# Optimization experiments

Hardware: AMD Instinct MI355X
Metric: run time of the kernel (lower is better)

Reference implementation:

```python
import jax, jax.numpy as jnp
import numpy as np

N_NODES = 100000
N_EDGES = 1600000
N_GRAPHS = 1024
IN_CH = 64
HID = 32
H4, H2 = HID * 4, HID * 2


def _glorot(key, shape):
    fan_in, fan_out = shape[0], shape[1]
    lim = (6.0 / (fan_in + fan_out)) ** 0.5
    return jax.random.uniform(key, shape, jnp.float32, -lim, lim)


def setup_inputs() -> dict:
    key = jax.random.key(0)
    ks = jax.random.split(key, 32)
    inp = {
        "x": jax.random.normal(ks[0], (N_NODES, IN_CH), jnp.float32),
        "edge_index": jax.random.randint(ks[1], (2, N_EDGES), 0, N_NODES, jnp.int64),
        "batch": jnp.sort(jax.random.randint(ks[2], (N_NODES,), 0, N_GRAPHS, jnp.int64)),
    }
    dims = [(IN_CH, H4), (H4, H2), (H2, H2), (H2, H2)]
    for i, (di, do) in enumerate(dims, 1):
        inp[f"c{i}_wl"] = _glorot(ks[3 * i], (di, do))
        inp[f"c{i}_bl"] = jnp.zeros((do,), jnp.float32)
        inp[f"c{i}_wr"] = _glorot(ks[3 * i + 1], (di, do))
    lin_dims = [(H2, H2), (H2, HID), (HID, HID), (HID, 1)]
    for i, (di, do) in enumerate(lin_dims, 1):
        inp[f"lin{i}_w"] = _glorot(ks[15 + 2 * i], (di, do))
        inp[f"lin{i}_b"] = jnp.zeros((do,), jnp.float32)
    return inp


def _sage(x, src, dst, wl, bl, wr):
    # mean-aggregate neighbor (source) features at target nodes
    agg = jax.ops.segment_sum(x[src], dst, num_segments=N_NODES)
    deg = jax.ops.segment_sum(jnp.ones((src.shape[0],), x.dtype), dst, num_segments=N_NODES)
    agg = agg / jnp.maximum(deg, 1.0)[:, None]
    return agg @ wl + bl + x @ wr


def reference(x, edge_index, batch,
              c1_wl, c1_bl, c1_wr, c2_wl, c2_bl, c2_wr,
              c3_wl, c3_bl, c3_wr, c4_wl, c4_bl, c4_wr,
              lin1_w, lin1_b, lin2_w, lin2_b, lin3_w, lin3_b, lin4_w, lin4_b):
    src, dst = edge_index[0], edge_index[1]
    h = jax.nn.relu(_sage(x, src, dst, c1_wl, c1_bl, c1_wr))
    h = jax.nn.relu(_sage(h, src, dst, c2_wl, c2_bl, c2_wr))
    h = jax.nn.relu(_sage(h, src, dst, c3_wl, c3_bl, c3_wr))
    h = jax.nn.relu(_sage(h, src, dst, c4_wl, c4_bl, c4_wr))
    # global mean pool over graphs
    gsum = jax.ops.segment_sum(h, batch, num_segments=N_GRAPHS)
    gcnt = jax.ops.segment_sum(jnp.ones((h.shape[0],), h.dtype), batch, num_segments=N_GRAPHS)
    g = gsum / jnp.maximum(gcnt, 1.0)[:, None]
    g = jax.nn.relu(g @ lin1_w + lin1_b)
    g = jax.nn.relu(g @ lin2_w + lin2_b)
    g = jax.nn.relu(g @ lin3_w + lin3_b)
    out = (g @ lin4_w + lin4_b).squeeze(1)  # [N_GRAPHS]
    return out
```

## Files before the change

kernel.cpp:

```cpp
#include <hip/hip_runtime.h>

#define NN 100000
#define NE 1600000
#define NG 1024
#define NBLK_SCAN ((NN + 255) / 256)
#define NPART 2

#define CPAD 16

#define GB_COUNT 6250
#define GB_CVT   3125
#define GB_BND   5
#define GB_PREP  320
#define GB_SETUP (GB_COUNT + GB_CVT + GB_BND + GB_PREP)

typedef __attribute__((ext_vector_type(8))) short bf16x8;
typedef __attribute__((ext_vector_type(4))) float f32x4;

__device__ __forceinline__ unsigned f2bf1(float f) {
  union { float f; unsigned u; } v; v.f = f;
  return (v.u + 0x7fffu + ((v.u >> 16) & 1u)) >> 16;
}
__device__ __forceinline__ unsigned packbf2(float a, float b) {
  return f2bf1(a) | (f2bf1(b) << 16);
}
__device__ __forceinline__ float bflo(unsigned u) {
  union { unsigned u; float f; } v; v.u = u << 16; return v.f;
}
__device__ __forceinline__ float bfhi(unsigned u) {
  union { unsigned u; float f; } v; v.u = u & 0xffff0000u; return v.f;
}
__device__ __forceinline__ float bfs(unsigned short s) {
  union { unsigned u; float f; } v; v.u = ((unsigned)s) << 16; return v.f;
}

__global__ __launch_bounds__(256) void k_setup(
    const int* __restrict__ dst, int* __restrict__ cnt, int* __restrict__ rank,
    const float* __restrict__ X, unsigned short* __restrict__ Xb,
    const int* __restrict__ batch, int* __restrict__ gstart,
    const float* __restrict__ c1wl, const float* __restrict__ c1wr,
    const float* __restrict__ c2wl, const float* __restrict__ c2wr,
    const float* __restrict__ c3wl, const float* __restrict__ c3wr,
    const float* __restrict__ c4wl, const float* __restrict__ c4wr,
    unsigned short* __restrict__ pL1, unsigned short* __restrict__ pL2a,
    unsigned short* __restrict__ pL2b, unsigned short* __restrict__ pL3,
    unsigned short* __restrict__ pL4) {
  int b = blockIdx.x, tid = threadIdx.x;
  if (b < GB_COUNT) {
    int e = b * 256 + tid;
    rank[e] = atomicAdd(&cnt[(size_t)dst[e] * CPAD], 1);
    return;
  }
  b -= GB_COUNT;
  if (b < GB_CVT) {
    int i = b * 256 + tid;
    const float4* p = (const float4*)X + (size_t)i * 2;
    float4 a = p[0], c = p[1];
    uint4 o;
    o.x = packbf2(a.x, a.y); o.y = packbf2(a.z, a.w);
    o.z = packbf2(c.x, c.y); o.w = packbf2(c.z, c.w);
    ((uint4*)Xb)[i] = o;
    return;
  }
  b -= GB_CVT;
  if (b < GB_BND) {
    int g = b * 256 + tid;
    if (g > NG) return;
    int lo = 0, hi = NN;
    while (lo < hi) {
      int mid = (lo + hi) >> 1;
      if (batch[mid] < g) lo = mid + 1; else hi = mid;
    }
    gstart[g] = lo;
    return;
  }
  b -= GB_BND;
  {
    int yb = b >> 6, xb = b & 63;
    const float *WL, *WR; unsigned short* dstp; int N;
    if (yb == 0)      { WL = c1wl; WR = c1wr;           dstp = pL1;  N = 128; }
    else if (yb == 1) { WL = c2wl; WR = c2wl + 64 * 64; dstp = pL2a; N = 64; }
    else if (yb == 2) { WL = c2wr; WR = c2wr + 64 * 64; dstp = pL2b; N = 64; }
    else if (yb == 3) { WL = c3wl; WR = c3wr;           dstp = pL3;  N = 64; }
    else              { WL = c4wl; WR = c4wr;           dstp = pL4;  N = 64; }
    int e = xb * 256 + tid;
    if (e >= 128 * N) return;
    int k = e / N, n = e - k * N;
    float w = (k < 64) ? WL[k * N + n] : WR[(k - 64) * N + n];
    int t = k >> 5, kq = (k >> 3) & 3, j = k & 7;
    int n0 = n >> 4, nl = n & 15;
    dstp[((((n0 * 4 + t) * 64) + (kq * 16 + nl)) << 3) + j] =
        (unsigned short)f2bf1(w);
  }
}

__global__ __launch_bounds__(256) void k_scan1(const int* __restrict__ cnt,
                                               int* __restrict__ off,
                                               int* __restrict__ bsum) {
  __shared__ int s[256];
  int tid = threadIdx.x;
  int i = blockIdx.x * 256 + tid;
  int v = (i < NN) ? cnt[(size_t)i * CPAD] : 0;
  s[tid] = v;
  __syncthreads();
  for (int d = 1; d < 256; d <<= 1) {
    int t = (tid >= d) ? s[tid - d] : 0;
    __syncthreads();
    s[tid] += t;
    __syncthreads();
  }
  if (i < NN) off[i] = s[tid] - v;
  if (tid == 255) bsum[blockIdx.x] = s[255];
}

__global__ __launch_bounds__(256) void k_scan23(int* __restrict__ off,
                                                const int* __restrict__ bsum,
                                                const int* __restrict__ cnt,
                                                float* __restrict__ inv) {
  __shared__ int red[256];
  int b = blockIdx.x, tid = threadIdx.x;
  int s = 0;
  for (int j = tid; j < b; j += 256) s += bsum[j];
  red[tid] = s;
  __syncthreads();
  for (int d = 128; d > 0; d >>= 1) {
    if (tid < d) red[tid] += red[tid + d];
    __syncthreads();
  }
  int base = red[0];
  int i = b * 256 + tid;
  if (i < NN) {
    off[i] = off[i] + base;
    inv[i] = 1.0f / fmaxf((float)cnt[(size_t)i * CPAD], 1.0f);
  }
  if (i == 0) off[NN] = NE;
}

__global__ __launch_bounds__(256) void k_fill(const int* __restrict__ src,
                                              const int* __restrict__ dst,
                                              const int* __restrict__ off,
                                              const int* __restrict__ rank,
                                              int* __restrict__ csr) {
  int e = blockIdx.x * 256 + threadIdx.x;
  int lo = (int)blockIdx.y * (NN / NPART);
  int hi = lo + (NN / NPART);
  if (e < NE) {
    int d = dst[e];
    if (d >= lo && d < hi) csr[off[d] + rank[e]] = src[e];
  }
}

__global__ __launch_bounds__(256) void k_gather(
    const unsigned short* __restrict__ F, const int* __restrict__ csr,
    const int* __restrict__ off, const float* __restrict__ inv,
    const float* __restrict__ bias, const unsigned short* __restrict__ Z,
    unsigned short* __restrict__ out) {
  int idx = blockIdx.x * 256 + threadIdx.x;
  int n = idx >> 3, q = idx & 7;
  int beg = off[n], end = off[n + 1];
  float aA[8], aB[8];
#pragma unroll
  for (int c = 0; c < 8; ++c) { aA[c] = 0.f; aB[c] = 0.f; }
  int e = beg;
  for (; e + 4 <= end; e += 4) {
    uint4 v[4];
#pragma unroll
    for (int j = 0; j < 4; ++j)
      v[j] = ((const uint4*)(F + (size_t)csr[e + j] * 64))[q];
#pragma unroll
    for (int j = 0; j < 4; j += 2) {
      aA[0] += bflo(v[j].x); aB[0] += bflo(v[j + 1].x);
      aA[1] += bfhi(v[j].x); aB[1] += bfhi(v[j + 1].x);
      aA[2] += bflo(v[j].y); aB[2] += bflo(v[j + 1].y);
      aA[3] += bfhi(v[j].y); aB[3] += bfhi(v[j + 1].y);
      aA[4] += bflo(v[j].z); aB[4] += bflo(v[j + 1].z);
      aA[5] += bfhi(v[j].z); aB[5] += bfhi(v[j + 1].z);
      aA[6] += bflo(v[j].w); aB[6] += bflo(v[j + 1].w);
      aA[7] += bfhi(v[j].w); aB[7] += bfhi(v[j + 1].w);
    }
  }
  for (; e < end; ++e) {
    uint4 v0 = ((const uint4*)(F + (size_t)csr[e] * 64))[q];
    aA[0] += bflo(v0.x); aA[1] += bfhi(v0.x);
    aA[2] += bflo(v0.y); aA[3] += bfhi(v0.y);
    aA[4] += bflo(v0.z); aA[5] += bfhi(v0.z);
    aA[6] += bflo(v0.w); aA[7] += bfhi(v0.w);
  }
  float a[8];
  float iv = inv[n];
#pragma unroll
  for (int c = 0; c < 8; ++c) a[c] = (aA[c] + aB[c]) * iv;
  {
    uint4 z = ((const uint4*)(Z + (size_t)n * 64))[q];
    const float4* bp = (const float4*)(bias + q * 8);
    float4 b0 = bp[0], b1 = bp[1];
    a[0] = fmaxf(a[0] + b0.x + bflo(z.x), 0.f);
    a[1] = fmaxf(a[1] + b0.y + bfhi(z.x), 0.f);
    a[2] = fmaxf(a[2] + b0.z + bflo(z.y), 0.f);
    a[3] = fmaxf(a[3] + b0.w + bfhi(z.y), 0.f);
    a[4] = fmaxf(a[4] + b1.x + bflo(z.z), 0.f);
    a[5] = fmaxf(a[5] + b1.y + bfhi(z.z), 0.f);
    a[6] = fmaxf(a[6] + b1.z + bflo(z.w), 0.f);
    a[7] = fmaxf(a[7] + b1.w + bfhi(z.w), 0.f);
  }
  uint4 o;
  o.x = packbf2(a[0], a[1]); o.y = packbf2(a[2], a[3]);
  o.z = packbf2(a[4], a[5]); o.w = packbf2(a[6], a[7]);
  ((uint4*)(out + (size_t)n * 64))[q] = o;
}

template <int NF>
__global__ __launch_bounds__(256, 4) void k_fgemm(
    const unsigned short* __restrict__ F, const int* __restrict__ csr,
    const int* __restrict__ off, const float* __restrict__ inv,
    const unsigned short* __restrict__ Wp, const float* __restrict__ bias,
    unsigned short* __restrict__ OUT, int outStride) {
  __shared__ __align__(16) char smem[64 * 66 * 4];
  unsigned short* sA = (unsigned short*)smem;
  float* sC = (float*)smem;
  const int tid = threadIdx.x;
  const int m0 = blockIdx.x * 64;

  {
    int m = tid >> 2, qr = tid & 3;
    int row = m0 + m;
    float a0[16], a1[16];
#pragma unroll
    for (int c = 0; c < 16; ++c) { a0[c] = 0.f; a1[c] = 0.f; }
    if (row < NN) {
      int beg = off[row], end = off[row + 1];
      int e = beg;
      for (; e + 2 <= end; e += 2) {
        int s0 = csr[e], s1 = csr[e + 1];
        const uint4* r0 = (const uint4*)(F + (size_t)s0 * 64) + qr * 2;
        const uint4* r1 = (const uint4*)(F + (size_t)s1 * 64) + qr * 2;
        uint4 p0 = r0[0], p1 = r0[1], q0 = r1[0], q1 = r1[1];
        a0[0] += bflo(p0.x); a0[1] += bfhi(p0.x);
        a0[2] += bflo(p0.y); a0[3] += bfhi(p0.y);
        a0[4] += bflo(p0.z); a0[5] += bfhi(p0.z);
        a0[6] += bflo(p0.w); a0[7] += bfhi(p0.w);
        a0[8] += bflo(p1.x); a0[9] += bfhi(p1.x);
        a0[10] += bflo(p1.y); a0[11] += bfhi(p1.y);
        a0[12] += bflo(p1.z); a0[13] += bfhi(p1.z);
        a0[14] += bflo(p1.w); a0[15] += bfhi(p1.w);
        a1[0] += bflo(q0.x); a1[1] += bfhi(q0.x);
        a1[2] += bflo(q0.y); a1[3] += bfhi(q0.y);
        a1[4] += bflo(q0.z); a1[5] += bfhi(q0.z);
        a1[6] += bflo(q0.w); a1[7] += bfhi(q0.w);
        a1[8] += bflo(q1.x); a1[9] += bfhi(q1.x);
        a1[10] += bflo(q1.y); a1[11] += bfhi(q1.y);
        a1[12] += bflo(q1.z); a1[13] += bfhi(q1.z);
        a1[14] += bflo(q1.w); a1[15] += bfhi(q1.w);
      }
      if (e < end) {
        const uint4* r0 = (const uint4*)(F + (size_t)csr[e] * 64) + qr * 2;
        uint4 p0 = r0[0], p1 = r0[1];
        a0[0] += bflo(p0.x); a0[1] += bfhi(p0.x);
        a0[2] += bflo(p0.y); a0[3] += bfhi(p0.y);
        a0[4] += bflo(p0.z); a0[5] += bfhi(p0.z);
        a0[6] += bflo(p0.w); a0[7] += bfhi(p0.w);
        a0[8] += bflo(p1.x); a0[9] += bfhi(p1.x);
        a0[10] += bflo(p1.y); a0[11] += bfhi(p1.y);
        a0[12] += bflo(p1.z); a0[13] += bfhi(p1.z);
        a0[14] += bflo(p1.w); a0[15] += bfhi(p1.w);
      }
      float iv = inv[row];
#pragma unroll
      for (int c = 0; c < 16; ++c) a0[c] = (a0[c] + a1[c]) * iv;
    } else {
#pragma unroll
      for (int c = 0; c < 16; ++c) a0[c] = 0.f;
    }
    int wv = m >> 4, mr = m & 15;
#pragma unroll
    for (int h = 0; h < 2; ++h) {
      int k8 = qr * 2 + h;
      int t = k8 >> 2, kq = k8 & 3;
      uint4 o;
      o.x = packbf2(a0[h * 8 + 0], a0[h * 8 + 1]);
      o.y = packbf2(a0[h * 8 + 2], a0[h * 8 + 3]);
      o.z = packbf2(a0[h * 8 + 4], a0[h * 8 + 5]);
      o.w = packbf2(a0[h * 8 + 6], a0[h * 8 + 7]);
      ((uint4*)sA)[(wv * 4 + t) * 64 + kq * 16 + mr] = o;
    }
  }
#pragma unroll
  for (int l = 0; l < 2; ++l) {
    int c = tid + l * 256;
    int m = c >> 3, j = c & 7;
    int row = m0 + m;
    uint4 v = make_uint4(0, 0, 0, 0);
    if (row < NN) v = ((const uint4*)(F + (size_t)row * 64))[j];
    int k8 = 8 + j, t = k8 >> 2, kq = k8 & 3;
    int wv = m >> 4, mr = m & 15;
    ((uint4*)sA)[(wv * 4 + t) * 64 + kq * 16 + mr] = v;
  }
  __syncthreads();

  const int w = tid >> 6, L = tid & 63;
  const bf16x8* Af = (const bf16x8*)sA;
  const bf16x8* Bf = (const bf16x8*)Wp;
  f32x4 acc[NF];
#pragma unroll
  for (int i = 0; i < NF; ++i)
#pragma unroll
    for (int j = 0; j < 4; ++j) acc[i][j] = 0.f;
#pragma unroll
  for (int t = 0; t < 4; ++t) {
    bf16x8 afr = Af[(w * 4 + t) * 64 + L];
#pragma unroll
    for (int n0 = 0; n0 < NF; ++n0) {
      bf16x8 bfr = Bf[(n0 * 4 + t) * 64 + L];
      acc[n0] = __builtin_amdgcn_mfma_f32_16x16x32_bf16(afr, bfr, acc[n0], 0, 0, 0);
    }
  }

  int rg = L >> 4, cl = L & 15;
#pragma unroll
  for (int half = 0; half < NF / 4; ++half) {
    __syncthreads();
#pragma unroll
    for (int n0 = 0; n0 < 4; ++n0)
#pragma unroll
      for (int r = 0; r < 4; ++r)
        sC[(w * 16 + rg * 4 + r) * 66 + n0 * 16 + cl] = acc[half * 4 + n0][r];
    __syncthreads();
#pragma unroll
    for (int it = 0; it < 2; ++it) {
      int c = tid + it * 256;
      int m = c >> 3, c8 = c & 7;
      int row = m0 + m;
      if (row < NN) {
        float v[8];
#pragma unroll
        for (int j = 0; j < 8; ++j)
          v[j] = fmaxf(sC[m * 66 + c8 * 8 + j] + bias[half * 64 + c8 * 8 + j], 0.f);
        uint4 o;
        o.x = packbf2(v[0], v[1]); o.y = packbf2(v[2], v[3]);
        o.z = packbf2(v[4], v[5]); o.w = packbf2(v[6], v[7]);
        ((uint4*)(OUT + (size_t)row * outStride + half * 64))[c8] = o;
      }
    }
  }
}

__global__ __launch_bounds__(256) void k_gemm(
    const unsigned short* __restrict__ S0,
    const unsigned short* __restrict__ Wp,
    const unsigned short* __restrict__ Wp2, unsigned short* __restrict__ OUT2,
    unsigned short* __restrict__ OUT, int M) {
  __shared__ __align__(16) char smem[64 * 66 * 4];
  unsigned short* sA = (unsigned short*)smem;
  float* sC = (float*)smem;
  const int tid = threadIdx.x;
  if (blockIdx.y == 1) { Wp = Wp2; OUT = OUT2; }
  const int m0 = blockIdx.x * 64;

#pragma unroll
  for (int l = 0; l < 4; ++l) {
    int c = tid + l * 256;
    int m = c >> 4, k8 = c & 15;
    int row = m0 + m;
    uint4 v = make_uint4(0, 0, 0, 0);
    if (row < M) v = ((const uint4*)(S0 + (size_t)row * 128))[k8];
    int wv = m >> 4, mr = m & 15, t = k8 >> 2, kq = k8 & 3;
    ((uint4*)sA)[(wv * 4 + t) * 64 + (kq * 16 + mr)] = v;
  }
  __syncthreads();

  const int w = tid >> 6, L = tid & 63;
  f32x4 acc[4];
#pragma unroll
  for (int i = 0; i < 4; ++i)
#pragma unroll
    for (int j = 0; j < 4; ++j) acc[i][j] = 0.f;

  const bf16x8* Af = (const bf16x8*)sA;
  const bf16x8* Bf = (const bf16x8*)Wp;
#pragma unroll
  for (int t = 0; t < 4; ++t) {
    bf16x8 afr = Af[(w * 4 + t) * 64 + L];
#pragma unroll
    for (int n0 = 0; n0 < 4; ++n0) {
      bf16x8 bfr = Bf[(n0 * 4 + t) * 64 + L];
      acc[n0] = __builtin_amdgcn_mfma_f32_16x16x32_bf16(afr, bfr, acc[n0], 0, 0, 0);
    }
  }
  __syncthreads();
  {
    int rg = L >> 4, cl = L & 15;
#pragma unroll
    for (int n0 = 0; n0 < 4; ++n0)
#pragma unroll
      for (int r = 0; r < 4; ++r)
        sC[(w * 16 + rg * 4 + r) * 66 + n0 * 16 + cl] = acc[n0][r];
  }
  __syncthreads();
#pragma unroll
  for (int it = 0; it < 2; ++it) {
    int c = tid + it * 256;
    int m = c >> 3, c8 = c & 7;
    int row = m0 + m;
    if (row < M) {
      float v[8];
#pragma unroll
      for (int j = 0; j < 8; ++j) v[j] = sC[m * 66 + c8 * 8 + j];
      uint4 o;
      o.x = packbf2(v[0], v[1]); o.y = packbf2(v[2], v[3]);
      o.z = packbf2(v[4], v[5]); o.w = packbf2(v[6], v[7]);
      ((uint4*)(OUT + (size_t)row * 64))[c8] = o;
    }
  }
}

__global__ __launch_bounds__(64) void k_poolmlp(
    const unsigned short* __restrict__ H, const int* __restrict__ gstart,
    const float* __restrict__ w1, const float* __restrict__ b1,
    const float* __restrict__ w2, const float* __restrict__ b2,
    const float* __restrict__ w3, const float* __restrict__ b3,
    const float* __restrict__ w4, const float* __restrict__ b4,
    float* __restrict__ out) {
  __shared__ float sg[64], s1[64], s2[32], s3[32];
  int g = blockIdx.x, t = threadIdx.x;
  int beg = gstart[g], end = gstart[g + 1];
  float acc = 0.0f;
#pragma unroll 4
  for (int n = beg; n < end; ++n) acc += bfs(H[(size_t)n * 64 + t]);
  float cnt = fmaxf((float)(end - beg), 1.0f);
  sg[t] = acc / cnt;
  __syncthreads();
  acc = b1[t];
  for (int k = 0; k < 64; ++k) acc += sg[k] * w1[k * 64 + t];
  s1[t] = fmaxf(acc, 0.0f);
  __syncthreads();
  if (t < 32) {
    acc = b2[t];
    for (int k = 0; k < 64; ++k) acc += s1[k] * w2[k * 32 + t];
    s2[t] = fmaxf(acc, 0.0f);
  }
  __syncthreads();
  if (t < 32) {
    acc = b3[t];
    for (int k = 0; k < 32; ++k) acc += s2[k] * w3[k * 32 + t];
    s3[t] = fmaxf(acc, 0.0f);
  }
  __syncthreads();
  if (t == 0) {
    acc = b4[0];
    for (int k = 0; k < 32; ++k) acc += s3[k] * w4[k];
    out[g] = acc;
  }
}

extern "C" void kernel_launch(void* const* d_in, const int* in_sizes, int n_in,
                              void* d_out, int out_size, void* d_ws,
                              size_t ws_size, hipStream_t stream) {
  const float* x     = (const float*)d_in[0];
  const int*   ei    = (const int*)d_in[1];
  const int*   batch = (const int*)d_in[2];
  const int* src = ei;
  const int* dst = ei + NE;

  const float* c1_wl = (const float*)d_in[3];
  const float* c1_bl = (const float*)d_in[4];
  const float* c1_wr = (const float*)d_in[5];
  const float* c2_wl = (const float*)d_in[6];
  const float* c2_bl = (const float*)d_in[7];
  const float* c2_wr = (const float*)d_in[8];
  const float* c3_wl = (const float*)d_in[9];
  const float* c3_bl = (const float*)d_in[10];
  const float* c3_wr = (const float*)d_in[11];
  const float* c4_wl = (const float*)d_in[12];
  const float* c4_bl = (const float*)d_in[13];
  const float* c4_wr = (const float*)d_in[14];
  const float* l1w = (const float*)d_in[15];
  const float* l1b = (const float*)d_in[16];
  const float* l2w = (const float*)d_in[17];
  const float* l2b = (const float*)d_in[18];
  const float* l3w = (const float*)d_in[19];
  const float* l3b = (const float*)d_in[20];
  const float* l4w = (const float*)d_in[21];
  const float* l4b = (const float*)d_in[22];

  char* wsb = (char*)d_ws;
  float* inv = (float*)wsb;
  unsigned short* xb  = (unsigned short*)(wsb + (size_t)NN * 4);
  unsigned short* B1  = xb + (size_t)NN * 64;
  unsigned short* B2  = B1 + (size_t)NN * 64;
  unsigned short* B3  = B2 + (size_t)NN * 128;
  unsigned short* B4  = B3 + (size_t)NN * 64;
  unsigned short* pL1  = B4 + (size_t)NN * 64;
  unsigned short* pL2a = pL1 + 128 * 128;
  unsigned short* pL2b = pL2a + 128 * 64;
  unsigned short* pL3  = pL2b + 128 * 64;
  unsigned short* pL4  = pL3 + 128 * 64;
  int* cnt    = (int*)(pL4 + 128 * 64);
  int* off    = cnt + (size_t)NN * CPAD;
  int* bsum   = off + NN + 1;
  int* gstart = bsum + 512;
  int* csr    = gstart + NG + 1 + 2;
  int* rank   = csr + NE;

  const int gE  = (NE + 255) / 256;
  const int gN8 = NN * 8 / 256;
  const int gM  = (NN + 63) / 64;
  const int gN  = NBLK_SCAN;

  hipMemsetAsync(cnt, 0, (size_t)NN * CPAD * 4, stream);

  k_setup<<<GB_SETUP, 256, 0, stream>>>(dst, cnt, rank, x, xb, batch, gstart,
                                        c1_wl, c1_wr, c2_wl, c2_wr,
                                        c3_wl, c3_wr, c4_wl, c4_wr,
                                        pL1, pL2a, pL2b, pL3, pL4);
  k_scan1<<<gN, 256, 0, stream>>>(cnt, off, bsum);
  k_scan23<<<gN, 256, 0, stream>>>(off, bsum, cnt, inv);
  k_fill<<<dim3(gE, NPART), 256, 0, stream>>>(src, dst, off, rank, csr);

  k_fgemm<8><<<gM, 256, 0, stream>>>(xb, csr, off, inv, pL1, c1_bl, B2, 128);

  k_gemm<<<dim3(gM, 2), 256, 0, stream>>>(B2, pL2a, pL2b, B4, B3, NN);
  k_gather<<<gN8, 256, 0, stream>>>(B3, csr, off, inv, c2_bl, B4, B1);

  k_fgemm<4><<<gM, 256, 0, stream>>>(B1, csr, off, inv, pL3, c3_bl, B3, 64);

  k_fgemm<4><<<gM, 256, 0, stream>>>(B3, csr, off, inv, pL4, c4_bl, B1, 64);

  k_poolmlp<<<NG, 64, 0, stream>>>(B1, gstart, l1w, l1b, l2w, l2b,
                                   l3w, l3b, l4w, l4b, (float*)d_out);
}
```

Measured before the change: 406.7 us.

## Precompute layer-1 root GEMM inside setup, interleaved with edge counting

```diff
diff --git a/kernel.cpp b/kernel.cpp
--- a/kernel.cpp
+++ b/kernel.cpp
@@ -5,14 +5,14 @@
 #define NG 1024
 #define NBLK_SCAN ((NN + 255) / 256)
 #define NPART 2
-
-#define CPAD 16
+#define CPAD 4
 
 #define GB_COUNT 6250
+#define GB_Z     1563
 #define GB_CVT   3125
 #define GB_BND   5
 #define GB_PREP  320
-#define GB_SETUP (GB_COUNT + GB_CVT + GB_BND + GB_PREP)
+#define GB_SETUP (2 * GB_COUNT)
 
 typedef __attribute__((ext_vector_type(8))) short bf16x8;
 typedef __attribute__((ext_vector_type(4))) float f32x4;
@@ -32,12 +32,25 @@
 }
 __device__ __forceinline__ float bfs(unsigned short s) {
   union { unsigned u; float f; } v; v.u = ((unsigned)s) << 16; return v.f;
+}
+
+__global__ __launch_bounds__(256) void k_prepz(const float* __restrict__ c1wr,
+                                               unsigned short* __restrict__ pLZ) {
+  int e = blockIdx.x * 256 + threadIdx.x;
+  if (e >= 64 * 128) return;
+  int k = e >> 7, n = e & 127;
+  int t = k >> 5, kq = (k >> 3) & 3, j = k & 7;
+  int n0 = n >> 4, nl = n & 15;
+  pLZ[((((n0 * 2 + t) * 64) + (kq * 16 + nl)) << 3) + j] =
+      (unsigned short)f2bf1(c1wr[k * 128 + n]);
 }
 
 __global__ __launch_bounds__(256) void k_setup(
     const int* __restrict__ dst, int* __restrict__ cnt, int* __restrict__ rank,
     const float* __restrict__ X, unsigned short* __restrict__ Xb,
     const int* __restrict__ batch, int* __restrict__ gstart,
+    const unsigned short* __restrict__ pLZ, const float* __restrict__ c1bl,
+    unsigned short* __restrict__ ZZ,
     const float* __restrict__ c1wl, const float* __restrict__ c1wr,
     const float* __restrict__ c2wl, const float* __restrict__ c2wr,
     const float* __restrict__ c3wl, const float* __restrict__ c3wr,
@@ -45,15 +58,85 @@
     unsigned short* __restrict__ pL1, unsigned short* __restrict__ pL2a,
     unsigned short* __restrict__ pL2b, unsigned short* __restrict__ pL3,
     unsigned short* __restrict__ pL4) {
+  __shared__ __align__(16) char smem[64 * 66 * 4];
   int b = blockIdx.x, tid = threadIdx.x;
-  if (b < GB_COUNT) {
-    int e = b * 256 + tid;
+
+  if ((b & 1) == 0) {
+    int e = (b >> 1) * 256 + tid;
     rank[e] = atomicAdd(&cnt[(size_t)dst[e] * CPAD], 1);
     return;
   }
-  b -= GB_COUNT;
-  if (b < GB_CVT) {
-    int i = b * 256 + tid;
+  int ob = b >> 1;
+
+  if (ob < GB_Z) {
+    unsigned short* sA = (unsigned short*)smem;
+    float* sC = (float*)smem;
+    const int m0 = ob * 64;
+#pragma unroll
+    for (int l = 0; l < 2; ++l) {
+      int c = tid + l * 256;
+      int m = c >> 3, k8 = c & 7;
+      int row = m0 + m;
+      uint4 o = make_uint4(0, 0, 0, 0);
+      if (row < NN) {
+        const float4* xp = (const float4*)(X + (size_t)row * 64 + k8 * 8);
+        float4 p0 = xp[0], p1 = xp[1];
+        o.x = packbf2(p0.x, p0.y); o.y = packbf2(p0.z, p0.w);
+        o.z = packbf2(p1.x, p1.y); o.w = packbf2(p1.z, p1.w);
+      }
+      int wv = m >> 4, mr = m & 15, t = k8 >> 2, kq = k8 & 3;
+      ((uint4*)sA)[(wv * 2 + t) * 64 + kq * 16 + mr] = o;
+    }
+    __syncthreads();
+    const int w = tid >> 6, L = tid & 63;
+    const bf16x8* Af = (const bf16x8*)sA;
+    const bf16x8* Bf = (const bf16x8*)pLZ;
+    f32x4 acc[8];
+#pragma unroll
+    for (int i = 0; i < 8; ++i)
+#pragma unroll
+      for (int j = 0; j < 4; ++j) acc[i][j] = 0.f;
+#pragma unroll
+    for (int t = 0; t < 2; ++t) {
+      bf16x8 afr = Af[(w * 2 + t) * 64 + L];
+#pragma unroll
+      for (int n0 = 0; n0 < 8; ++n0) {
+        bf16x8 bfr = Bf[(n0 * 2 + t) * 64 + L];
+        acc[n0] = __builtin_amdgcn_mfma_f32_16x16x32_bf16(afr, bfr, acc[n0], 0, 0, 0);
+      }
+    }
+    int rg = L >> 4, cl = L & 15;
+#pragma unroll
+    for (int half = 0; half < 2; ++half) {
+      __syncthreads();
+#pragma unroll
+      for (int n0 = 0; n0 < 4; ++n0)
+#pragma unroll
+        for (int r = 0; r < 4; ++r)
+          sC[(w * 16 + rg * 4 + r) * 66 + n0 * 16 + cl] = acc[half * 4 + n0][r];
+      __syncthreads();
+#pragma unroll
+      for (int it = 0; it < 2; ++it) {
+        int c = tid + it * 256;
+        int m = c >> 3, c8 = c & 7;
+        int row = m0 + m;
+        if (row < NN) {
+          float v[8];
+#pragma unroll
+          for (int j = 0; j < 8; ++j)
+            v[j] = sC[m * 66 + c8 * 8 + j] + c1bl[half * 64 + c8 * 8 + j];
+          uint4 o;
+          o.x = packbf2(v[0], v[1]); o.y = packbf2(v[2], v[3]);
+          o.z = packbf2(v[4], v[5]); o.w = packbf2(v[6], v[7]);
+          ((uint4*)(ZZ + (size_t)row * 128 + half * 64))[c8] = o;
+        }
+      }
+    }
+    return;
+  }
+  ob -= GB_Z;
+  if (ob < GB_CVT) {
+    int i = ob * 256 + tid;
     const float4* p = (const float4*)X + (size_t)i * 2;
     float4 a = p[0], c = p[1];
     uint4 o;
@@ -62,9 +145,9 @@
     ((uint4*)Xb)[i] = o;
     return;
   }
-  b -= GB_CVT;
-  if (b < GB_BND) {
-    int g = b * 256 + tid;
+  ob -= GB_CVT;
+  if (ob < GB_BND) {
+    int g = ob * 256 + tid;
     if (g > NG) return;
     int lo = 0, hi = NN;
     while (lo < hi) {
@@ -74,9 +157,9 @@
     gstart[g] = lo;
     return;
   }
-  b -= GB_BND;
-  {
-    int yb = b >> 6, xb = b & 63;
+  ob -= GB_BND;
+  if (ob < GB_PREP) {
+    int yb = ob >> 6, xb = ob & 63;
     const float *WL, *WR; unsigned short* dstp; int N;
     if (yb == 0)      { WL = c1wl; WR = c1wr;           dstp = pL1;  N = 128; }
     else if (yb == 1) { WL = c2wl; WR = c2wl + 64 * 64; dstp = pL2a; N = 64; }
@@ -209,12 +292,12 @@
   ((uint4*)(out + (size_t)n * 64))[q] = o;
 }
 
-template <int NF>
-__global__ __launch_bounds__(256, 4) void k_fgemm(
+__global__ __launch_bounds__(256, 4) void k_fgemm1(
     const unsigned short* __restrict__ F, const int* __restrict__ csr,
     const int* __restrict__ off, const float* __restrict__ inv,
-    const unsigned short* __restrict__ Wp, const float* __restrict__ bias,
-    unsigned short* __restrict__ OUT, int outStride) {
+    const unsigned short* __restrict__ Wp,
+    const unsigned short* __restrict__ ZZ,
+    unsigned short* __restrict__ OUT) {
   __shared__ __align__(16) char smem[64 * 66 * 4];
   unsigned short* sA = (unsigned short*)smem;
   float* sC = (float*)smem;
@@ -267,9 +350,130 @@
       float iv = inv[row];
 #pragma unroll
       for (int c = 0; c < 16; ++c) a0[c] = (a0[c] + a1[c]) * iv;
-    } else {
-#pragma unroll
-      for (int c = 0; c < 16; ++c) a0[c] = 0.f;
+    }
+    int wv = m >> 4, mr = m & 15;
+#pragma unroll
+    for (int h = 0; h < 2; ++h) {
+      int k8 = qr * 2 + h;
+      int t = k8 >> 2, kq = k8 & 3;
+      uint4 o;
+      o.x = packbf2(a0[h * 8 + 0], a0[h * 8 + 1]);
+      o.y = packbf2(a0[h * 8 + 2], a0[h * 8 + 3]);
+      o.z = packbf2(a0[h * 8 + 4], a0[h * 8 + 5]);
+      o.w = packbf2(a0[h * 8 + 6], a0[h * 8 + 7]);
+      ((uint4*)sA)[(wv * 2 + t) * 64 + kq * 16 + mr] = o;
+    }
+  }
+  __syncthreads();
+
+  const int w = tid >> 6, L = tid & 63;
+  const bf16x8* Af = (const bf16x8*)sA;
+  const bf16x8* Bf = (const bf16x8*)Wp;
+  f32x4 acc[8];
+#pragma unroll
+  for (int i = 0; i < 8; ++i)
+#pragma unroll
+    for (int j = 0; j < 4; ++j) acc[i][j] = 0.f;
+#pragma unroll
+  for (int t = 0; t < 2; ++t) {
+    bf16x8 afr = Af[(w * 2 + t) * 64 + L];
+#pragma unroll
+    for (int n0 = 0; n0 < 8; ++n0) {
+      bf16x8 bfr = Bf[(n0 * 4 + t) * 64 + L];
+      acc[n0] = __builtin_amdgcn_mfma_f32_16x16x32_bf16(afr, bfr, acc[n0], 0, 0, 0);
+    }
+  }
+
+  int rg = L >> 4, cl = L & 15;
+#pragma unroll
+  for (int half = 0; half < 2; ++half) {
+    __syncthreads();
+#pragma unroll
+    for (int n0 = 0; n0 < 4; ++n0)
+#pragma unroll
+      for (int r = 0; r < 4; ++r)
+        sC[(w * 16 + rg * 4 + r) * 66 + n0 * 16 + cl] = acc[half * 4 + n0][r];
+    __syncthreads();
+#pragma unroll
+    for (int it = 0; it < 2; ++it) {
+      int c = tid + it * 256;
+      int m = c >> 3, c8 = c & 7;
+      int row = m0 + m;
+      if (row < NN) {
+        uint4 z = ((const uint4*)(ZZ + (size_t)row * 128 + half * 64))[c8];
+        float zb[8] = {bflo(z.x), bfhi(z.x), bflo(z.y), bfhi(z.y),
+                       bflo(z.z), bfhi(z.z), bflo(z.w), bfhi(z.w)};
+        float v[8];
+#pragma unroll
+        for (int j = 0; j < 8; ++j)
+          v[j] = fmaxf(sC[m * 66 + c8 * 8 + j] + zb[j], 0.f);
+        uint4 o;
+        o.x = packbf2(v[0], v[1]); o.y = packbf2(v[2], v[3]);
+        o.z = packbf2(v[4], v[5]); o.w = packbf2(v[6], v[7]);
+        ((uint4*)(OUT + (size_t)row * 128 + half * 64))[c8] = o;
+      }
+    }
+  }
+}
+
+template <int NF>
+__global__ __launch_bounds__(256, 4) void k_fgemm(
+    const unsigned short* __restrict__ F, const int* __restrict__ csr,
+    const int* __restrict__ off, const float* __restrict__ inv,
+    const unsigned short* __restrict__ Wp, const float* __restrict__ bias,
+    unsigned short* __restrict__ OUT, int outStride) {
+  __shared__ __align__(16) char smem[64 * 66 * 4];
+  unsigned short* sA = (unsigned short*)smem;
+  float* sC = (float*)smem;
+  const int tid = threadIdx.x;
+  const int m0 = blockIdx.x * 64;
+
+  {
+    int m = tid >> 2, qr = tid & 3;
+    int row = m0 + m;
+    float a0[16], a1[16];
+#pragma unroll
+    for (int c = 0; c < 16; ++c) { a0[c] = 0.f; a1[c] = 0.f; }
+    if (row < NN) {
+      int beg = off[row], end = off[row + 1];
+      int e = beg;
+      for (; e + 2 <= end; e += 2) {
+        int s0 = csr[e], s1 = csr[e + 1];
+        const uint4* r0 = (const uint4*)(F + (size_t)s0 * 64) + qr * 2;
+        const uint4* r1 = (const uint4*)(F + (size_t)s1 * 64) + qr * 2;
+        uint4 p0 = r0[0], p1 = r0[1], q0 = r1[0], q1 = r1[1];
+        a0[0] += bflo(p0.x); a0[1] += bfhi(p0.x);
+        a0[2] += bflo(p0.y); a0[3] += bfhi(p0.y);
+        a0[4] += bflo(p0.z); a0[5] += bfhi(p0.z);
+        a0[6] += bflo(p0.w); a0[7] += bfhi(p0.w);
+        a0[8] += bflo(p1.x); a0[9] += bfhi(p1.x);
+        a0[10] += bflo(p1.y); a0[11] += bfhi(p1.y);
+        a0[12] += bflo(p1.z); a0[13] += bfhi(p1.z);
+        a0[14] += bflo(p1.w); a0[15] += bfhi(p1.w);
+        a1[0] += bflo(q0.x); a1[1] += bfhi(q0.x);
+        a1[2] += bflo(q0.y); a1[3] += bfhi(q0.y);
+        a1[4] += bflo(q0.z); a1[5] += bfhi(q0.z);
+        a1[6] += bflo(q0.w); a1[7] += bfhi(q0.w);
+        a1[8] += bflo(q1.x); a1[9] += bfhi(q1.x);
+        a1[10] += bflo(q1.y); a1[11] += bfhi(q1.y);
+        a1[12] += bflo(q1.z); a1[13] += bfhi(q1.z);
+        a1[14] += bflo(q1.w); a1[15] += bfhi(q1.w);
+      }
+      if (e < end) {
+        const uint4* r0 = (const uint4*)(F + (size_t)csr[e] * 64) + qr * 2;
+        uint4 p0 = r0[0], p1 = r0[1];
+        a0[0] += bflo(p0.x); a0[1] += bfhi(p0.x);
+        a0[2] += bflo(p0.y); a0[3] += bfhi(p0.y);
+        a0[4] += bflo(p0.z); a0[5] += bfhi(p0.z);
+        a0[6] += bflo(p0.w); a0[7] += bfhi(p0.w);
+        a0[8] += bflo(p1.x); a0[9] += bfhi(p1.x);
+        a0[10] += bflo(p1.y); a0[11] += bfhi(p1.y);
+        a0[12] += bflo(p1.z); a0[13] += bfhi(p1.z);
+        a0[14] += bflo(p1.w); a0[15] += bfhi(p1.w);
+      }
+      float iv = inv[row];
+#pragma unroll
+      for (int c = 0; c < 16; ++c) a0[c] = (a0[c] + a1[c]) * iv;
     }
     int wv = m >> 4, mr = m & 15;
 #pragma unroll
@@ -489,12 +693,14 @@
   unsigned short* B2  = B1 + (size_t)NN * 64;
   unsigned short* B3  = B2 + (size_t)NN * 128;
   unsigned short* B4  = B3 + (size_t)NN * 64;
-  unsigned short* pL1  = B4 + (size_t)NN * 64;
+  unsigned short* ZZ  = B4 + (size_t)NN * 64;
+  unsigned short* pL1  = ZZ + (size_t)NN * 128;
   unsigned short* pL2a = pL1 + 128 * 128;
   unsigned short* pL2b = pL2a + 128 * 64;
   unsigned short* pL3  = pL2b + 128 * 64;
   unsigned short* pL4  = pL3 + 128 * 64;
-  int* cnt    = (int*)(pL4 + 128 * 64);
+  unsigned short* pLZ  = pL4 + 128 * 64;
+  int* cnt    = (int*)(pLZ + 64 * 128);
   int* off    = cnt + (size_t)NN * CPAD;
   int* bsum   = off + NN + 1;
   int* gstart = bsum + 512;
@@ -508,7 +714,10 @@
 
   hipMemsetAsync(cnt, 0, (size_t)NN * CPAD * 4, stream);
 
+  k_prepz<<<32, 256, 0, stream>>>(c1_wr, pLZ);
+
   k_setup<<<GB_SETUP, 256, 0, stream>>>(dst, cnt, rank, x, xb, batch, gstart,
+                                        pLZ, c1_bl, ZZ,
                                         c1_wl, c1_wr, c2_wl, c2_wr,
                                         c3_wl, c3_wr, c4_wl, c4_wr,
                                         pL1, pL2a, pL2b, pL3, pL4);
@@ -516,7 +725,7 @@
   k_scan23<<<gN, 256, 0, stream>>>(off, bsum, cnt, inv);
   k_fill<<<dim3(gE, NPART), 256, 0, stream>>>(src, dst, off, rank, csr);
 
-  k_fgemm<8><<<gM, 256, 0, stream>>>(xb, csr, off, inv, pL1, c1_bl, B2, 128);
+  k_fgemm1<<<gM, 256, 0, stream>>>(xb, csr, off, inv, pL1, ZZ, B2);
 
   k_gemm<<<dim3(gM, 2), 256, 0, stream>>>(B2, pL2a, pL2b, B4, B3, NN);
   k_gather<<<gN8, 256, 0, stream>>>(B3, csr, off, inv, c2_bl, B4, B1);
```

Result: no change. 402.0 us (-1.2%).
